# Performance work log

Hardware: AMD Instinct MI355X
Metric: run time of the kernel (lower is better)

Reference implementation:

```python
import jax, jax.numpy as jnp
import numpy as np

N, E = 50000, 800000
IN_CH, HID, OUT = 128, 64, 64
H1, H2 = 4, 1
NEG_SLOPE = 0.2  # PyG GATConv default


def _glorot(key, shape):
    fan_in, fan_out = shape[0], shape[-1]
    lim = (6.0 / (fan_in + fan_out)) ** 0.5
    return jax.random.uniform(key, shape, jnp.float32, -lim, lim)


def setup_inputs() -> dict:
    key = jax.random.key(0)
    ks = jax.random.split(key, 12)
    x = jax.random.normal(ks[0], (N, IN_CH), jnp.float32)
    edge_index = jax.random.randint(ks[1], (2, E), 0, N, jnp.int64)
    # layer 1: in_ch -> hid, 4 heads, concat
    W1 = _glorot(ks[2], (IN_CH, H1 * HID))
    a_src1 = _glorot(ks[3], (H1, HID))
    a_dst1 = _glorot(ks[4], (H1, HID))
    b1 = jnp.zeros((H1 * HID,), jnp.float32)
    # layer 2: hid*4 -> out, 1 head, mean (concat=False)
    W2 = _glorot(ks[5], (H1 * HID, H2 * OUT))
    a_src2 = _glorot(ks[6], (H2, OUT))
    a_dst2 = _glorot(ks[7], (H2, OUT))
    b2 = jnp.zeros((OUT,), jnp.float32)
    return {"x": x, "edge_index": edge_index, "W1": W1, "a_src1": a_src1,
            "a_dst1": a_dst1, "b1": b1, "W2": W2, "a_src2": a_src2,
            "a_dst2": a_dst2, "b2": b2}


def gat_layer(x, src, dst, W, a_src, a_dst, b, concat):
    n = x.shape[0]
    Hh, Fh = a_src.shape
    h = (x @ W).reshape(n, Hh, Fh)                      # [N,H,F]
    al_src = jnp.sum(h * a_src[None], axis=-1)          # [N,H]
    al_dst = jnp.sum(h * a_dst[None], axis=-1)          # [N,H]
    logits = jax.nn.leaky_relu(al_src[src] + al_dst[dst], NEG_SLOPE)  # [E,H]
    # numerically stable segment softmax over destination nodes
    mx = jax.ops.segment_max(logits, dst, num_segments=n)
    mx = jnp.where(jnp.isfinite(mx), mx, 0.0)
    e = jnp.exp(logits - mx[dst])                       # [E,H]
    denom = jax.ops.segment_sum(e, dst, num_segments=n)  # [N,H]
    alpha = e / jnp.maximum(denom[dst], 1e-16)          # [E,H]
    msg = h[src] * alpha[:, :, None]                    # [E,H,F]
    out = jax.ops.segment_sum(msg, dst, num_segments=n)  # [N,H,F]
    out = out.reshape(n, Hh * Fh) if concat else out.mean(axis=1)
    return out + b


def reference(x, edge_index, W1, a_src1, a_dst1, b1, W2, a_src2, a_dst2, b2):
    n = x.shape[0]
    # PyG GATConv adds self-loops by default
    loops = jnp.arange(n, dtype=edge_index.dtype)
    src = jnp.concatenate([edge_index[0], loops])
    dst = jnp.concatenate([edge_index[1], loops])
    h = gat_layer(x, src, dst, W1, a_src1, a_dst1, b1, concat=True)
    h = jax.nn.elu(h)
    # dropout is identity in eval mode
    out = gat_layer(h, src, dst, W2, a_src2, a_dst2, b2, concat=False)
    return out
```

## Files before the change

kernel.cpp:

```cpp
#include <hip/hip_runtime.h>
#include <math.h>

#define NEG_SLOPE 0.2f
#define SLOTS 64
#define PARTB 256

typedef unsigned short ushort_t;
typedef _Float16 f16x8 __attribute__((ext_vector_type(8)));
typedef _Float16 h2v  __attribute__((ext_vector_type(2)));
typedef float f32x4v __attribute__((ext_vector_type(4)));

__device__ __forceinline__ float leaky(float x) { return x > 0.f ? x : NEG_SLOPE * x; }

__device__ __forceinline__ ushort_t f2h(float f) {
    union { _Float16 h; ushort_t u; } v; v.h = (_Float16)f; return v.u;
}
__device__ __forceinline__ unsigned packh(float a, float b) {
    union { h2v h; unsigned u; } c; c.h[0] = (_Float16)a; c.h[1] = (_Float16)b; return c.u;
}

__global__ __launch_bounds__(256) void k_prep0(const float* __restrict__ W1, const float* __restrict__ W2,
                                               const float* __restrict__ as1, const float* __restrict__ ad1,
                                               const float* __restrict__ as2, const float* __restrict__ ad2,
                                               ushort_t* __restrict__ W1t, ushort_t* __restrict__ W2t,
                                               float* __restrict__ va1s, float* __restrict__ va1d,
                                               float* __restrict__ va2s, float* __restrict__ va2d) {
    int b = blockIdx.x, t = threadIdx.x;
    if (b < 256) {
        if (t < 128) W1t[b * 128 + t] = f2h(W1[t * 256 + b]);
    } else if (b < 320) {
        int n = b - 256;
        W2t[n * 256 + t] = f2h(W2[t * 64 + n]);
    } else if (b == 320) {
        for (int idx = t; idx < 1024; idx += 256) {
            int k = idx >> 3, h = (idx >> 1) & 3, sd = idx & 1;
            const float* a = sd ? ad1 : as1;
            float acc = 0.f;
            for (int f = 0; f < 64; ++f) acc += W1[k * 256 + h * 64 + f] * a[h * 64 + f];
            (sd ? va1d : va1s)[k * 4 + h] = acc;
        }
    } else {
        for (int idx = t; idx < 512; idx += 256) {
            int k = idx >> 1, sd = idx & 1;
            const float* a = sd ? ad2 : as2;
            float acc = 0.f;
            for (int f = 0; f < 64; ++f) acc += W2[k * 64 + f] * a[f];
            (sd ? va2d : va2s)[k] = acc;
        }
    }
}

__global__ __launch_bounds__(256) void k_partA(const int* __restrict__ ei, int E, int CH, int NBKT,
                                               int* __restrict__ bcnt) {
    __shared__ int hist[256];
    int k = blockIdx.x, t = threadIdx.x;
    hist[t] = 0;
    __syncthreads();
    int i0 = k * CH;
    for (int it = 0; it < CH; it += 256) {
        int i = i0 + it + t;
        if (it + t < CH && i < E) {
            int d = ei[E + i];
            atomicAdd(&hist[d >> 8], 1);
        }
    }
    __syncthreads();
    if (t < NBKT) bcnt[t * PARTB + k] = hist[t];
}

__global__ __launch_bounds__(256) void k_partB1(const int* __restrict__ bcnt,
                                                int* __restrict__ offs, int* __restrict__ btot) {
    __shared__ int wsum[4];
    int t = threadIdx.x, b = blockIdx.x;
    int c = bcnt[b * PARTB + t];
    int lane = t & 63, w = t >> 6;
    int v = c;
    #pragma unroll
    for (int off = 1; off < 64; off <<= 1) {
        int u = __shfl_up(v, off, 64);
        if (lane >= off) v += u;
    }
    if (lane == 63) wsum[w] = v;
    __syncthreads();
    int add = 0;
    for (int ww = 0; ww < w; ++ww) add += wsum[ww];
    offs[b * PARTB + t] = v - c + add;
    if (t == 255) btot[b] = v + add;
}

__global__ __launch_bounds__(256) void k_partB2(const int* __restrict__ btot,
                                                int* __restrict__ bstart, int NBKT, int E) {
    __shared__ int wsum[4];
    int t = threadIdx.x;
    int c = (t < NBKT) ? btot[t] : 0;
    int lane = t & 63, w = t >> 6;
    int v = c;
    #pragma unroll
    for (int off = 1; off < 64; off <<= 1) {
        int u = __shfl_up(v, off, 64);
        if (lane >= off) v += u;
    }
    if (lane == 63) wsum[w] = v;
    __syncthreads();
    int add = 0;
    for (int ww = 0; ww < w; ++ww) add += wsum[ww];
    if (t < NBKT) bstart[t] = v - c + add;
    if (t == 0) bstart[NBKT] = E;
}

__global__ __launch_bounds__(256) void k_partC(const int* __restrict__ ei, int E, int CH, int NBKT,
                                               const int* __restrict__ offs, const int* __restrict__ bstart,
                                               unsigned* __restrict__ epk) {
    __shared__ int cur[256];
    int k = blockIdx.x, t = threadIdx.x;
    if (t < NBKT) cur[t] = bstart[t] + offs[t * PARTB + k];
    __syncthreads();
    int i0 = k * CH;
    for (int it = 0; it < CH; it += 256) {
        int i = i0 + it + t;
        if (it + t < CH && i < E) {
            unsigned s = (unsigned)ei[i];
            unsigned d = (unsigned)ei[E + i];
            int pos = atomicAdd(&cur[d >> 8], 1);
            epk[pos] = (d << 16) | s;
        }
    }
}

__global__ __launch_bounds__(256) void k_partD(const unsigned* __restrict__ epk, const int* __restrict__ bstart,
                                               int* __restrict__ cnt, ushort_t* __restrict__ csr, int N) {
    __shared__ ushort_t rows[256 * SLOTS];
    __shared__ int cl[256];
    int b = blockIdx.x, t = threadIdx.x;
    for (int i = t; i < 256 * SLOTS / 8; i += 256)
        *(uint4*)&rows[(size_t)i * 8] = make_uint4(0, 0, 0, 0);
    cl[t] = 0;
    __syncthreads();
    int n0 = b * 256;
    if (n0 + t < N) rows[t * SLOTS] = (ushort_t)(n0 + t);
    int e0 = bstart[b], e1 = bstart[b + 1];
    for (int i = e0 + t; i < e1; i += 256) {
        unsigned u = epk[i];
        int dl = (u >> 16) & 255;
        int slot = atomicAdd(&cl[dl], 1);
        if (slot < SLOTS - 1) rows[dl * SLOTS + 1 + slot] = (ushort_t)(u & 0xFFFFu);
    }
    __syncthreads();
    int nvalid = N - n0; if (nvalid > 256) nvalid = 256;
    size_t gbase = (size_t)n0 * SLOTS;
    for (int i = t; i < nvalid * SLOTS / 8; i += 256)
        *(uint4*)(csr + gbase + (size_t)i * 8) = *(const uint4*)&rows[(size_t)i * 8];
    if (t < nvalid) {
        int c = cl[t]; if (c > SLOTS - 1) c = SLOTS - 1;
        cnt[n0 + t] = c;
    }
}

__global__ __launch_bounds__(256) void k_prep1x(const float* __restrict__ x,
                                                const float* __restrict__ va1s, const float* __restrict__ va1d,
                                                ushort_t* __restrict__ xh,
                                                float4* __restrict__ alS, float4* __restrict__ alD, int N) {
    int b = blockIdx.x, t = threadIdx.x;
    int r = b * 16 + (t >> 4);
    int idx = t & 15;
    if (r >= N) return;
    const float* xr = x + (size_t)r * 128 + idx * 8;
    float4 f0 = *(const float4*)xr;
    float4 f1 = *(const float4*)(xr + 4);
    uint4 pv;
    pv.x = packh(f0.x, f0.y); pv.y = packh(f0.z, f0.w);
    pv.z = packh(f1.x, f1.y); pv.w = packh(f1.z, f1.w);
    *(uint4*)&xh[(size_t)r * 128 + idx * 8] = pv;
    float xs[8] = {f0.x, f0.y, f0.z, f0.w, f1.x, f1.y, f1.z, f1.w};
    float s0 = 0, s1 = 0, s2 = 0, s3 = 0, d0 = 0, d1 = 0, d2 = 0, d3 = 0;
    #pragma unroll
    for (int j = 0; j < 8; ++j) {
        int k = idx * 8 + j;
        float4 vs = *(const float4*)&va1s[k * 4];
        float4 vd = *(const float4*)&va1d[k * 4];
        s0 += xs[j] * vs.x; s1 += xs[j] * vs.y; s2 += xs[j] * vs.z; s3 += xs[j] * vs.w;
        d0 += xs[j] * vd.x; d1 += xs[j] * vd.y; d2 += xs[j] * vd.z; d3 += xs[j] * vd.w;
    }
    #pragma unroll
    for (int off = 8; off >= 1; off >>= 1) {
        s0 += __shfl_xor(s0, off, 64); s1 += __shfl_xor(s1, off, 64);
        s2 += __shfl_xor(s2, off, 64); s3 += __shfl_xor(s3, off, 64);
        d0 += __shfl_xor(d0, off, 64); d1 += __shfl_xor(d1, off, 64);
        d2 += __shfl_xor(d2, off, 64); d3 += __shfl_xor(d3, off, 64);
    }
    if (idx == 0) {
        alS[r] = make_float4(s0, s1, s2, s3);
        alD[r] = make_float4(d0, d1, d2, d3);
    }
}

#define CONS(p, a) do { \
    _Float16 ah_ = (_Float16)(a); \
    h2v a2_ = {ah_, ah_}; \
    union { uint4 u; h2v h[4]; } c_; c_.u = (p); \
    ha0 += c_.h[0] * a2_; ha1 += c_.h[1] * a2_; \
    ha2 += c_.h[2] * a2_; ha3 += c_.h[3] * a2_; } while (0)

#define FLUSH() do { \
    acc[0] += (float)ha0[0]; acc[1] += (float)ha0[1]; \
    acc[2] += (float)ha1[0]; acc[3] += (float)ha1[1]; \
    acc[4] += (float)ha2[0]; acc[5] += (float)ha2[1]; \
    acc[6] += (float)ha3[0]; acc[7] += (float)ha3[1]; \
    ha0 = (h2v)0; ha1 = (h2v)0; ha2 = (h2v)0; ha3 = (h2v)0; } while (0)

__global__ __launch_bounds__(256) void k_agg1(const int* __restrict__ cnt, const ushort_t* __restrict__ csr,
                                              const float4* __restrict__ alS4, const float4* __restrict__ alD4,
                                              const ushort_t* __restrict__ xh,
                                              ushort_t* __restrict__ aggh, int N) {
    __shared__ float s_alpha[4][SLOTS][4];
    __shared__ int   s_off[4][SLOTS];
    int w = threadIdx.x >> 6, lane = threadIdx.x & 63;
    int n = blockIdx.x * 4 + w;
    if (n >= N) return;
    int stored = cnt[n]; if (stored > SLOTS - 1) stored = SLOTS - 1;
    int deg = stored + 1;
    int s = 0;
    if (lane < deg) s = csr[(size_t)n * SLOTS + lane];
    s_off[w][lane] = (lane < deg) ? (s << 8) : 0;

    float e0 = 0.f, e1 = 0.f, e2 = 0.f, e3 = 0.f;
    if (lane < deg) {
        float4 ald = alD4[n];
        float4 as = alS4[s];
        e0 = __expf(leaky(as.x + ald.x));
        e1 = __expf(leaky(as.y + ald.y));
        e2 = __expf(leaky(as.z + ald.z));
        e3 = __expf(leaky(as.w + ald.w));
    }
    *(float4*)&s_alpha[w][lane][0] = make_float4(e0, e1, e2, e3);

    int head = lane >> 4, cid = lane & 15;
    const char* xb = (const char*)xh + cid * 16;

    float acc[8];
    #pragma unroll
    for (int i = 0; i < 8; ++i) acc[i] = 0.f;
    h2v ha0 = (h2v)0, ha1 = (h2v)0, ha2 = (h2v)0, ha3 = (h2v)0;

    int nit = (deg + 3) & ~3;

    int4 ovA = *(const int4*)&s_off[w][0];
    uint4 pA0 = *(const uint4*)(xb + ovA.x);
    uint4 pA1 = *(const uint4*)(xb + ovA.y);
    uint4 pA2 = *(const uint4*)(xb + ovA.z);
    uint4 pA3 = *(const uint4*)(xb + ovA.w);

    for (int j = 0; j < nit; j += 8) {
        uint4 pB0, pB1, pB2, pB3;
        bool hasB = (j + 4 < nit);
        if (hasB) {
            int4 ovB = *(const int4*)&s_off[w][j + 4];
            pB0 = *(const uint4*)(xb + ovB.x);
            pB1 = *(const uint4*)(xb + ovB.y);
            pB2 = *(const uint4*)(xb + ovB.z);
            pB3 = *(const uint4*)(xb + ovB.w);
        }
        {
            float a0 = s_alpha[w][j + 0][head];
            float a1 = s_alpha[w][j + 1][head];
            float a2 = s_alpha[w][j + 2][head];
            float a3 = s_alpha[w][j + 3][head];
            CONS(pA0, a0); CONS(pA1, a1); CONS(pA2, a2); CONS(pA3, a3);
        }
        if (hasB) {
            if (j + 8 < nit) {
                int4 ovA2 = *(const int4*)&s_off[w][j + 8];
                pA0 = *(const uint4*)(xb + ovA2.x);
                pA1 = *(const uint4*)(xb + ovA2.y);
                pA2 = *(const uint4*)(xb + ovA2.z);
                pA3 = *(const uint4*)(xb + ovA2.w);
            }
            float a0 = s_alpha[w][j + 4][head];
            float a1 = s_alpha[w][j + 5][head];
            float a2 = s_alpha[w][j + 6][head];
            float a3 = s_alpha[w][j + 7][head];
            CONS(pB0, a0); CONS(pB1, a1); CONS(pB2, a2); CONS(pB3, a3);
        }
        FLUSH();
    }

    float d0 = e0, d1 = e1, d2 = e2, d3 = e3;
    #pragma unroll
    for (int off = 32; off >= 1; off >>= 1) {
        d0 += __shfl_xor(d0, off, 64); d1 += __shfl_xor(d1, off, 64);
        d2 += __shfl_xor(d2, off, 64); d3 += __shfl_xor(d3, off, 64);
    }
    float dh = head == 0 ? d0 : head == 1 ? d1 : head == 2 ? d2 : d3;
    float inv = 1.f / fmaxf(dh, 1e-16f);

    uint4 u;
    u.x = packh(acc[0] * inv, acc[1] * inv);
    u.y = packh(acc[2] * inv, acc[3] * inv);
    u.z = packh(acc[4] * inv, acc[5] * inv);
    u.w = packh(acc[6] * inv, acc[7] * inv);
    *(uint4*)(aggh + (size_t)n * 512 + head * 128 + cid * 8) = u;
}
#undef CONS
#undef FLUSH

__global__ __launch_bounds__(256) void k_gemmO(const ushort_t* __restrict__ aggh, const ushort_t* __restrict__ W1t,
                                               const ushort_t* __restrict__ W2t,
                                               const float* __restrict__ b1,
                                               const float* __restrict__ va2s, const float* __restrict__ va2d,
                                               ushort_t* __restrict__ h2h,
                                               float* __restrict__ al2S, float* __restrict__ al2D, int N) {
    __shared__ ushort_t sU[4 * 32 * 136];
    __shared__ float s_al2w[4][32][2];
    int t = threadIdx.x;
    int w = t >> 6, lane = t & 63;
    int m = lane & 15, quad = lane >> 4;
    int r0 = blockIdx.x * 32;

    #pragma unroll
    for (int q = 0; q < 8; ++q) {
        int idx = t + q * 256;
        int row = idx >> 6, off = idx & 63;
        int gr = r0 + row;
        uint4 v = (gr < N) ? *(const uint4*)(aggh + (size_t)gr * 512 + off * 8)
                           : make_uint4(0, 0, 0, 0);
        int h = off >> 4, k8 = off & 15;
        *(uint4*)&sU[(size_t)(h * 32 + row) * 136 + k8 * 8] = v;
    }
    __syncthreads();

    f32x4v acc[2][4];
    #pragma unroll
    for (int r = 0; r < 2; ++r)
        #pragma unroll
        for (int cg = 0; cg < 4; ++cg) acc[r][cg] = (f32x4v){0.f, 0.f, 0.f, 0.f};
    #pragma unroll
    for (int ks = 0; ks < 4; ++ks) {
        f16x8 af[2];
        #pragma unroll
        for (int r = 0; r < 2; ++r)
            af[r] = *(f16x8*)&sU[(size_t)(w * 32 + r * 16 + m) * 136 + ks * 32 + quad * 8];
        #pragma unroll
        for (int cg = 0; cg < 4; ++cg) {
            f16x8 bf = *(f16x8*)&W1t[(size_t)(w * 64 + cg * 16 + m) * 128 + ks * 32 + quad * 8];
            #pragma unroll
            for (int r = 0; r < 2; ++r)
                acc[r][cg] = __builtin_amdgcn_mfma_f32_16x16x32_f16(af[r], bf, acc[r][cg], 0, 0, 0);
        }
    }
    __syncthreads();

    ushort_t* sO = sU;
    float ps[2][4], pd[2][4];
    #pragma unroll
    for (int r = 0; r < 2; ++r)
        #pragma unroll
        for (int reg = 0; reg < 4; ++reg) { ps[r][reg] = 0.f; pd[r][reg] = 0.f; }
    #pragma unroll
    for (int cg = 0; cg < 4; ++cg) {
        int c = w * 64 + cg * 16 + m;
        float bias = b1[c];
        float v2s = va2s[c], v2d = va2d[c];
        #pragma unroll
        for (int r = 0; r < 2; ++r)
            #pragma unroll
            for (int reg = 0; reg < 4; ++reg) {
                int row = r * 16 + quad * 4 + reg;
                float v = acc[r][cg][reg] + bias;
                v = v > 0.f ? v : (__expf(v) - 1.f);
                sO[(size_t)row * 264 + c] = f2h(v);
                ps[r][reg] += v * v2s;
                pd[r][reg] += v * v2d;
            }
    }
    #pragma unroll
    for (int off = 1; off <= 8; off <<= 1)
        #pragma unroll
        for (int r = 0; r < 2; ++r)
            #pragma unroll
            for (int reg = 0; reg < 4; ++reg) {
                ps[r][reg] += __shfl_xor(ps[r][reg], off, 64);
                pd[r][reg] += __shfl_xor(pd[r][reg], off, 64);
            }
    if (m == 0) {
        #pragma unroll
        for (int r = 0; r < 2; ++r)
            #pragma unroll
            for (int reg = 0; reg < 4; ++reg) {
                int row = r * 16 + quad * 4 + reg;
                s_al2w[w][row][0] = ps[r][reg];
                s_al2w[w][row][1] = pd[r][reg];
            }
    }
    __syncthreads();

    if (t < 32) {
        int gr = r0 + t;
        if (gr < N) {
            float a = 0.f, b = 0.f;
            #pragma unroll
            for (int w2 = 0; w2 < 4; ++w2) { a += s_al2w[w2][t][0]; b += s_al2w[w2][t][1]; }
            al2S[gr] = a; al2D[gr] = b;
        }
    }

    f32x4v acc2[2];
    #pragma unroll
    for (int r = 0; r < 2; ++r) acc2[r] = (f32x4v){0.f, 0.f, 0.f, 0.f};
    #pragma unroll
    for (int kb = 0; kb < 2; ++kb)
        #pragma unroll
        for (int ks = 0; ks < 4; ++ks) {
            int kk = kb * 128 + ks * 32 + quad * 8;
            f16x8 bf = *(f16x8*)&W2t[(size_t)(w * 16 + m) * 256 + kk];
            #pragma unroll
            for (int r = 0; r < 2; ++r) {
                f16x8 af = *(f16x8*)&sO[(size_t)(r * 16 + m) * 264 + kk];
                acc2[r] = __builtin_amdgcn_mfma_f32_16x16x32_f16(af, bf, acc2[r], 0, 0, 0);
            }
        }
    int col = w * 16 + m;
    #pragma unroll
    for (int r = 0; r < 2; ++r) {
        int gr0 = r0 + r * 16 + quad * 4;
        #pragma unroll
        for (int reg = 0; reg < 4; ++reg) {
            int gr = gr0 + reg;
            if (gr < N) h2h[(size_t)gr * 64 + col] = f2h(acc2[r][reg]);
        }
    }
}

__global__ __launch_bounds__(256) void k_agg2(const int* __restrict__ cnt, const ushort_t* __restrict__ csr,
                                              const float* __restrict__ alS, const float* __restrict__ alD,
                                              const ushort_t* __restrict__ h2h, const float* __restrict__ b2,
                                              float* __restrict__ out, int N) {
    int lane = threadIdx.x & 63;
    int n = blockIdx.x * 4 + (threadIdx.x >> 6);
    if (n >= N) return;
    int stored = cnt[n]; if (stored > SLOTS - 1) stored = SLOTS - 1;
    int deg = stored + 1;
    const ushort_t* crow = csr + (size_t)n * SLOTS;

    int s0 = 0;
    if (lane < deg) s0 = crow[lane];

    int grp = lane >> 3, cid = lane & 7;
    int choff = cid * 16;
    const char* hbase = (const char*)h2h;

    uint4 pbuf[3];
    #pragma unroll
    for (int i = 0; i < 3; ++i) {
        int sj = __shfl(s0, i * 8 + grp, 64);
        pbuf[i] = *(const uint4*)(hbase + ((size_t)sj << 7) + choff);
    }

    float ald = alD[n];
    float e0 = 0.f;
    if (lane < deg) e0 = __expf(leaky(alS[s0] + ald));

    h2v ha0 = (h2v)0, ha1 = (h2v)0, ha2 = (h2v)0, ha3 = (h2v)0;
    #pragma unroll
    for (int i = 0; i < 3; ++i) {
        float a = __shfl(e0, i * 8 + grp, 64);
        union { uint4 u; h2v h[4]; } c; c.u = pbuf[i];
        _Float16 ah = (_Float16)a;
        h2v a2 = {ah, ah};
        ha0 += c.h[0] * a2; ha1 += c.h[1] * a2;
        ha2 += c.h[2] * a2; ha3 += c.h[3] * a2;
    }
    for (int j = 24; j < deg; j += 8) {
        int jj = j + grp;
        float a = __shfl(e0, jj, 64);
        int sj = __shfl(s0, jj, 64);
        union { uint4 u; h2v h[4]; } c;
        c.u = *(const uint4*)(hbase + ((size_t)sj << 7) + choff);
        _Float16 ah = (_Float16)a;
        h2v a2 = {ah, ah};
        ha0 += c.h[0] * a2; ha1 += c.h[1] * a2;
        ha2 += c.h[2] * a2; ha3 += c.h[3] * a2;
    }

    float den = e0;
    #pragma unroll
    for (int off = 32; off >= 1; off >>= 1) den += __shfl_xor(den, off, 64);
    float inv = 1.f / fmaxf(den, 1e-16f);

    float acc[8];
    acc[0] = (float)ha0[0]; acc[1] = (float)ha0[1];
    acc[2] = (float)ha1[0]; acc[3] = (float)ha1[1];
    acc[4] = (float)ha2[0]; acc[5] = (float)ha2[1];
    acc[6] = (float)ha3[0]; acc[7] = (float)ha3[1];
    #pragma unroll
    for (int off = 8; off <= 32; off <<= 1)
        #pragma unroll
        for (int i = 0; i < 8; ++i) acc[i] += __shfl_xor(acc[i], off, 64);

    if (grp == 0) {
        int c8 = cid * 8;
        float4 b0 = *(const float4*)&b2[c8];
        float4 b1v = *(const float4*)&b2[c8 + 4];
        float4 o0 = make_float4(acc[0]*inv + b0.x, acc[1]*inv + b0.y, acc[2]*inv + b0.z, acc[3]*inv + b0.w);
        float4 o1 = make_float4(acc[4]*inv + b1v.x, acc[5]*inv + b1v.y, acc[6]*inv + b1v.z, acc[7]*inv + b1v.w);
        *(float4*)(out + (size_t)n * 64 + c8) = o0;
        *(float4*)(out + (size_t)n * 64 + c8 + 4) = o1;
    }
}

extern "C" void kernel_launch(void* const* d_in, const int* in_sizes, int n_in,
                              void* d_out, int out_size, void* d_ws, size_t ws_size,
                              hipStream_t stream) {
    const float* x      = (const float*)d_in[0];
    const int*   ei     = (const int*)d_in[1];
    const float* W1     = (const float*)d_in[2];
    const float* a_src1 = (const float*)d_in[3];
    const float* a_dst1 = (const float*)d_in[4];
    const float* b1     = (const float*)d_in[5];
    const float* W2     = (const float*)d_in[6];
    const float* a_src2 = (const float*)d_in[7];
    const float* a_dst2 = (const float*)d_in[8];
    const float* b2     = (const float*)d_in[9];
    float* out = (float*)d_out;

    int N = in_sizes[0] / 128;
    int E = in_sizes[1] / 2;

    char* ws = (char*)d_ws;
    size_t off = 0;
    auto alloc = [&](size_t bytes) -> void* {
        void* p = ws + off;
        off = (off + bytes + 255) & ~(size_t)255;
        return p;
    };
    ushort_t* xh    = (ushort_t*)alloc((size_t)N * 128 * 2);
    ushort_t* aggh  = (ushort_t*)alloc((size_t)N * 512 * 2);
    ushort_t* h2h   = (ushort_t*)alloc((size_t)N * 64 * 2);
    ushort_t* W1t   = (ushort_t*)alloc(256 * 128 * 2);
    ushort_t* W2t   = (ushort_t*)alloc(64 * 256 * 2);
    float* va1s  = (float*)alloc(128 * 4 * 4);
    float* va1d  = (float*)alloc(128 * 4 * 4);
    float* va2s  = (float*)alloc(256 * 4);
    float* va2d  = (float*)alloc(256 * 4);
    float* alS1  = (float*)alloc((size_t)N * 4 * 4);
    float* alD1  = (float*)alloc((size_t)N * 4 * 4);
    float* alS2  = (float*)alloc((size_t)N * 4);
    float* alD2  = (float*)alloc((size_t)N * 4);
    int*   cnt   = (int*)alloc((size_t)N * 4);
    ushort_t* csr = (ushort_t*)alloc((size_t)N * SLOTS * 2);
    int NBKT = (N + 255) >> 8;
    int*      bcnt  = (int*)alloc((size_t)NBKT * PARTB * 4);
    int*      offs  = (int*)alloc((size_t)NBKT * PARTB * 4);
    int*      btot  = (int*)alloc((size_t)NBKT * 4);
    int*      bstart= (int*)alloc((size_t)(NBKT + 1) * 4);
    unsigned* epk   = (unsigned*)alloc((size_t)E * 4);
    (void)ws_size; (void)n_in; (void)out_size;

    int CH  = (E + PARTB - 1) / PARTB;
    int XB  = (N + 15) / 16;
    int AB1 = (N + 3) / 4;
    int GO  = (N + 31) / 32;
    int NC4 = (N + 3) / 4;

    k_prep0<<<322, 256, 0, stream>>>(W1, W2, a_src1, a_dst1, a_src2, a_dst2,
                                     W1t, W2t, va1s, va1d, va2s, va2d);
    k_partA<<<PARTB, 256, 0, stream>>>(ei, E, CH, NBKT, bcnt);
    k_partB1<<<NBKT, 256, 0, stream>>>(bcnt, offs, btot);
    k_partB2<<<1, 256, 0, stream>>>(btot, bstart, NBKT, E);
    k_partC<<<PARTB, 256, 0, stream>>>(ei, E, CH, NBKT, offs, bstart, epk);
    k_partD<<<NBKT, 256, 0, stream>>>(epk, bstart, cnt, csr, N);
    k_prep1x<<<XB, 256, 0, stream>>>(x, va1s, va1d, xh, (float4*)alS1, (float4*)alD1, N);
    k_agg1<<<AB1, 256, 0, stream>>>(cnt, csr,
                                    (const float4*)alS1, (const float4*)alD1,
                                    xh, aggh, N);
    k_gemmO<<<GO, 256, 0, stream>>>(aggh, W1t, W2t, b1, va2s, va2d,
                                    h2h, alS2, alD2, N);
    k_agg2<<<NC4, 256, 0, stream>>>(cnt, csr, alS2, alD2, h2h, b2, out, N);
}
```

Measured before the change: 241.9 us.

## Merge independent prep kernels and split fused GEMM into two kernels

Merges the edge-histogram pass into the weight-prep kernel and the x-to-half/attention-logit pass into the edge-scatter kernel, so independent work shares launches and fills the GPU together. The fused layer-1 projection plus layer-2 GEMM kernel is split in two: the first writes the ELU output to a new global half buffer, and the second runs a separate 64-row tiled GEMM with W2 staged in shared memory. This removes launch gaps and may improve occupancy or tiling of the second GEMM, at the cost of an extra global round trip of N x 256 half values and one more launch.

```diff
diff --git a/kernel.cpp b/kernel.cpp
--- a/kernel.cpp
+++ b/kernel.cpp
@@ -19,13 +19,29 @@
     union { h2v h; unsigned u; } c; c.h[0] = (_Float16)a; c.h[1] = (_Float16)b; return c.u;
 }
 
-__global__ __launch_bounds__(256) void k_prep0(const float* __restrict__ W1, const float* __restrict__ W2,
-                                               const float* __restrict__ as1, const float* __restrict__ ad1,
-                                               const float* __restrict__ as2, const float* __restrict__ ad2,
-                                               ushort_t* __restrict__ W1t, ushort_t* __restrict__ W2t,
-                                               float* __restrict__ va1s, float* __restrict__ va1d,
-                                               float* __restrict__ va2s, float* __restrict__ va2d) {
+__global__ __launch_bounds__(256) void k_prep0A(const float* __restrict__ W1, const float* __restrict__ W2,
+                                                const float* __restrict__ as1, const float* __restrict__ ad1,
+                                                const float* __restrict__ as2, const float* __restrict__ ad2,
+                                                ushort_t* __restrict__ W1t, ushort_t* __restrict__ W2t,
+                                                float* __restrict__ va1s, float* __restrict__ va1d,
+                                                float* __restrict__ va2s, float* __restrict__ va2d,
+                                                const int* __restrict__ ei, int E, int CH, int NBKT,
+                                                int* __restrict__ bcnt) {
+    __shared__ int hist[256];
     int b = blockIdx.x, t = threadIdx.x;
+    if (b >= 322) {
+        int k = b - 322;
+        hist[t] = 0;
+        __syncthreads();
+        int i0 = k * CH;
+        for (int it = 0; it < CH; it += 256) {
+            int i = i0 + it + t;
+            if (it + t < CH && i < E) atomicAdd(&hist[ei[E + i] >> 8], 1);
+        }
+        __syncthreads();
+        if (t < NBKT) bcnt[t * PARTB + k] = hist[t];
+        return;
+    }
     if (b < 256) {
         if (t < 128) W1t[b * 128 + t] = f2h(W1[t * 256 + b]);
     } else if (b < 320) {
@@ -50,24 +66,6 @@
     }
 }
 
-__global__ __launch_bounds__(256) void k_partA(const int* __restrict__ ei, int E, int CH, int NBKT,
-                                               int* __restrict__ bcnt) {
-    __shared__ int hist[256];
-    int k = blockIdx.x, t = threadIdx.x;
-    hist[t] = 0;
-    __syncthreads();
-    int i0 = k * CH;
-    for (int it = 0; it < CH; it += 256) {
-        int i = i0 + it + t;
-        if (it + t < CH && i < E) {
-            int d = ei[E + i];
-            atomicAdd(&hist[d >> 8], 1);
-        }
-    }
-    __syncthreads();
-    if (t < NBKT) bcnt[t * PARTB + k] = hist[t];
-}
-
 __global__ __launch_bounds__(256) void k_partB1(const int* __restrict__ bcnt,
                                                 int* __restrict__ offs, int* __restrict__ btot) {
     __shared__ int wsum[4];
@@ -108,22 +106,62 @@
     if (t == 0) bstart[NBKT] = E;
 }
 
-__global__ __launch_bounds__(256) void k_partC(const int* __restrict__ ei, int E, int CH, int NBKT,
-                                               const int* __restrict__ offs, const int* __restrict__ bstart,
-                                               unsigned* __restrict__ epk) {
+__global__ __launch_bounds__(256) void k_partCx(const int* __restrict__ ei, int E, int CH, int NBKT,
+                                                const int* __restrict__ offs, const int* __restrict__ bstart,
+                                                unsigned* __restrict__ epk,
+                                                const float* __restrict__ x,
+                                                const float* __restrict__ va1s, const float* __restrict__ va1d,
+                                                ushort_t* __restrict__ xh,
+                                                float4* __restrict__ alS, float4* __restrict__ alD, int N) {
     __shared__ int cur[256];
-    int k = blockIdx.x, t = threadIdx.x;
-    if (t < NBKT) cur[t] = bstart[t] + offs[t * PARTB + k];
-    __syncthreads();
-    int i0 = k * CH;
-    for (int it = 0; it < CH; it += 256) {
-        int i = i0 + it + t;
-        if (it + t < CH && i < E) {
-            unsigned s = (unsigned)ei[i];
-            unsigned d = (unsigned)ei[E + i];
-            int pos = atomicAdd(&cur[d >> 8], 1);
-            epk[pos] = (d << 16) | s;
-        }
+    int b = blockIdx.x, t = threadIdx.x;
+    if (b < PARTB) {
+        int k = b;
+        if (t < NBKT) cur[t] = bstart[t] + offs[t * PARTB + k];
+        __syncthreads();
+        int i0 = k * CH;
+        for (int it = 0; it < CH; it += 256) {
+            int i = i0 + it + t;
+            if (it + t < CH && i < E) {
+                unsigned s = (unsigned)ei[i];
+                unsigned d = (unsigned)ei[E + i];
+                int pos = atomicAdd(&cur[d >> 8], 1);
+                epk[pos] = (d << 16) | s;
+            }
+        }
+        return;
+    }
+    int bb = b - PARTB;
+    int r = bb * 16 + (t >> 4);
+    int idx = t & 15;
+    if (r >= N) return;
+    const float* xr = x + (size_t)r * 128 + idx * 8;
+    float4 f0 = *(const float4*)xr;
+    float4 f1 = *(const float4*)(xr + 4);
+    uint4 pv;
+    pv.x = packh(f0.x, f0.y); pv.y = packh(f0.z, f0.w);
+    pv.z = packh(f1.x, f1.y); pv.w = packh(f1.z, f1.w);
+    *(uint4*)&xh[(size_t)r * 128 + idx * 8] = pv;
+    float xs[8] = {f0.x, f0.y, f0.z, f0.w, f1.x, f1.y, f1.z, f1.w};
+    float s0 = 0, s1 = 0, s2 = 0, s3 = 0, d0 = 0, d1 = 0, d2 = 0, d3 = 0;
+    #pragma unroll
+    for (int j = 0; j < 8; ++j) {
+        int k = idx * 8 + j;
+        float4 vs = *(const float4*)&va1s[k * 4];
+        float4 vd = *(const float4*)&va1d[k * 4];
+        s0 += xs[j] * vs.x; s1 += xs[j] * vs.y; s2 += xs[j] * vs.z; s3 += xs[j] * vs.w;
+        d0 += xs[j] * vd.x; d1 += xs[j] * vd.y; d2 += xs[j] * vd.z; d3 += xs[j] * vd.w;
+    }
+    #pragma unroll
+    for (int off = 8; off >= 1; off >>= 1) {
+        s0 += __shfl_xor(s0, off, 64); s1 += __shfl_xor(s1, off, 64);
+        s2 += __shfl_xor(s2, off, 64); s3 += __shfl_xor(s3, off, 64);
+        d0 += __shfl_xor(d0, off, 64); d1 += __shfl_xor(d1, off, 64);
+        d2 += __shfl_xor(d2, off, 64); d3 += __shfl_xor(d3, off, 64);
+    }
+    if (idx == 0) {
+        alS[r] = make_float4(s0, s1, s2, s3);
+        alD[r] = make_float4(d0, d1, d2, d3);
     }
 }
 
@@ -156,44 +194,6 @@
     }
 }
 
-__global__ __launch_bounds__(256) void k_prep1x(const float* __restrict__ x,
-                                                const float* __restrict__ va1s, const float* __restrict__ va1d,
-                                                ushort_t* __restrict__ xh,
-                                                float4* __restrict__ alS, float4* __restrict__ alD, int N) {
-    int b = blockIdx.x, t = threadIdx.x;
-    int r = b * 16 + (t >> 4);
-    int idx = t & 15;
-    if (r >= N) return;
-    const float* xr = x + (size_t)r * 128 + idx * 8;
-    float4 f0 = *(const float4*)xr;
-    float4 f1 = *(const float4*)(xr + 4);
-    uint4 pv;
-    pv.x = packh(f0.x, f0.y); pv.y = packh(f0.z, f0.w);
-    pv.z = packh(f1.x, f1.y); pv.w = packh(f1.z, f1.w);
-    *(uint4*)&xh[(size_t)r * 128 + idx * 8] = pv;
-    float xs[8] = {f0.x, f0.y, f0.z, f0.w, f1.x, f1.y, f1.z, f1.w};
-    float s0 = 0, s1 = 0, s2 = 0, s3 = 0, d0 = 0, d1 = 0, d2 = 0, d3 = 0;
-    #pragma unroll
-    for (int j = 0; j < 8; ++j) {
-        int k = idx * 8 + j;
-        float4 vs = *(const float4*)&va1s[k * 4];
-        float4 vd = *(const float4*)&va1d[k * 4];
-        s0 += xs[j] * vs.x; s1 += xs[j] * vs.y; s2 += xs[j] * vs.z; s3 += xs[j] * vs.w;
-        d0 += xs[j] * vd.x; d1 += xs[j] * vd.y; d2 += xs[j] * vd.z; d3 += xs[j] * vd.w;
-    }
-    #pragma unroll
-    for (int off = 8; off >= 1; off >>= 1) {
-        s0 += __shfl_xor(s0, off, 64); s1 += __shfl_xor(s1, off, 64);
-        s2 += __shfl_xor(s2, off, 64); s3 += __shfl_xor(s3, off, 64);
-        d0 += __shfl_xor(d0, off, 64); d1 += __shfl_xor(d1, off, 64);
-        d2 += __shfl_xor(d2, off, 64); d3 += __shfl_xor(d3, off, 64);
-    }
-    if (idx == 0) {
-        alS[r] = make_float4(s0, s1, s2, s3);
-        alD[r] = make_float4(d0, d1, d2, d3);
-    }
-}
-
 #define CONS(p, a) do { \
     _Float16 ah_ = (_Float16)(a); \
     h2v a2_ = {ah_, ah_}; \
@@ -303,12 +303,11 @@
 #undef CONS
 #undef FLUSH
 
-__global__ __launch_bounds__(256) void k_gemmO(const ushort_t* __restrict__ aggh, const ushort_t* __restrict__ W1t,
-                                               const ushort_t* __restrict__ W2t,
-                                               const float* __restrict__ b1,
-                                               const float* __restrict__ va2s, const float* __restrict__ va2d,
-                                               ushort_t* __restrict__ h2h,
-                                               float* __restrict__ al2S, float* __restrict__ al2D, int N) {
+__global__ __launch_bounds__(256) void k_g1(const ushort_t* __restrict__ aggh, const ushort_t* __restrict__ W1t,
+                                            const float* __restrict__ b1,
+                                            const float* __restrict__ va2s, const float* __restrict__ va2d,
+                                            ushort_t* __restrict__ out1h,
+                                            float* __restrict__ al2S, float* __restrict__ al2D, int N) {
     __shared__ ushort_t sU[4 * 32 * 136];
     __shared__ float s_al2w[4][32][2];
     int t = threadIdx.x;
@@ -347,9 +346,7 @@
                 acc[r][cg] = __builtin_amdgcn_mfma_f32_16x16x32_f16(af[r], bf, acc[r][cg], 0, 0, 0);
         }
     }
-    __syncthreads();
-
-    ushort_t* sO = sU;
+
     float ps[2][4], pd[2][4];
     #pragma unroll
     for (int r = 0; r < 2; ++r)
@@ -365,9 +362,10 @@
             #pragma unroll
             for (int reg = 0; reg < 4; ++reg) {
                 int row = r * 16 + quad * 4 + reg;
+                int gr = r0 + row;
                 float v = acc[r][cg][reg] + bias;
                 v = v > 0.f ? v : (__expf(v) - 1.f);
-                sO[(size_t)row * 264 + c] = f2h(v);
+                if (gr < N) out1h[(size_t)gr * 256 + c] = f2h(v);
                 ps[r][reg] += v * v2s;
                 pd[r][reg] += v * v2d;
             }
@@ -392,7 +390,6 @@
             }
     }
     __syncthreads();
-
     if (t < 32) {
         int gr = r0 + t;
         if (gr < N) {
@@ -402,30 +399,58 @@
             al2S[gr] = a; al2D[gr] = b;
         }
     }
-
-    f32x4v acc2[2];
-    #pragma unroll
-    for (int r = 0; r < 2; ++r) acc2[r] = (f32x4v){0.f, 0.f, 0.f, 0.f};
-    #pragma unroll
-    for (int kb = 0; kb < 2; ++kb)
+}
+
+__global__ __launch_bounds__(256) void k_g2(const ushort_t* __restrict__ in, const ushort_t* __restrict__ W2t,
+                                            ushort_t* __restrict__ h2h, int N) {
+    __shared__ ushort_t As[64 * 136];
+    __shared__ ushort_t Bs[64 * 136];
+    int t = threadIdx.x;
+    int r0 = blockIdx.x * 64;
+    int w = t >> 6, lane = t & 63;
+    int m = lane & 15, quad = lane >> 4;
+    f32x4v acc[4];
+    #pragma unroll
+    for (int r = 0; r < 4; ++r) acc[r] = (f32x4v){0.f, 0.f, 0.f, 0.f};
+    for (int kb = 0; kb < 2; ++kb) {
+        #pragma unroll
+        for (int q = 0; q < 4; ++q) {
+            int idx = t + q * 256;
+            int row = idx >> 4, off = idx & 15;
+            int gr = r0 + row;
+            uint4 v = (gr < N) ? *(const uint4*)(in + (size_t)gr * 256 + kb * 128 + off * 8)
+                               : make_uint4(0, 0, 0, 0);
+            *(uint4*)&As[row * 136 + off * 8] = v;
+        }
+        #pragma unroll
+        for (int q = 0; q < 4; ++q) {
+            int idx = t + q * 256;
+            int row = idx >> 4, off = idx & 15;
+            uint4 v = *(const uint4*)(W2t + (size_t)row * 256 + kb * 128 + off * 8);
+            *(uint4*)&Bs[row * 136 + off * 8] = v;
+        }
+        __syncthreads();
         #pragma unroll
         for (int ks = 0; ks < 4; ++ks) {
-            int kk = kb * 128 + ks * 32 + quad * 8;
-            f16x8 bf = *(f16x8*)&W2t[(size_t)(w * 16 + m) * 256 + kk];
+            int k0 = ks * 32 + quad * 8;
+            f16x8 af[4], bfr;
             #pragma unroll
-            for (int r = 0; r < 2; ++r) {
-                f16x8 af = *(f16x8*)&sO[(size_t)(r * 16 + m) * 264 + kk];
-                acc2[r] = __builtin_amdgcn_mfma_f32_16x16x32_f16(af, bf, acc2[r], 0, 0, 0);
-            }
-        }
+            for (int r = 0; r < 4; ++r) af[r] = *(f16x8*)&As[(r * 16 + m) * 136 + k0];
+            bfr = *(f16x8*)&Bs[(w * 16 + m) * 136 + k0];
+            #pragma unroll
+            for (int r = 0; r < 4; ++r)
+                acc[r] = __builtin_amdgcn_mfma_f32_16x16x32_f16(af[r], bfr, acc[r], 0, 0, 0);
+        }
+        __syncthreads();
+    }
     int col = w * 16 + m;
     #pragma unroll
-    for (int r = 0; r < 2; ++r) {
+    for (int r = 0; r < 4; ++r) {
         int gr0 = r0 + r * 16 + quad * 4;
         #pragma unroll
         for (int reg = 0; reg < 4; ++reg) {
             int gr = gr0 + reg;
-            if (gr < N) h2h[(size_t)gr * 64 + col] = f2h(acc2[r][reg]);
+            if (gr < N) h2h[(size_t)gr * 64 + col] = f2h(acc[r][reg]);
         }
     }
 }
@@ -534,6 +559,7 @@
     };
     ushort_t* xh    = (ushort_t*)alloc((size_t)N * 128 * 2);
     ushort_t* aggh  = (ushort_t*)alloc((size_t)N * 512 * 2);
+    ushort_t* out1h = (ushort_t*)alloc((size_t)N * 256 * 2);
     ushort_t* h2h   = (ushort_t*)alloc((size_t)N * 64 * 2);
     ushort_t* W1t   = (ushort_t*)alloc(256 * 128 * 2);
     ushort_t* W2t   = (ushort_t*)alloc(64 * 256 * 2);
@@ -558,21 +584,22 @@
     int CH  = (E + PARTB - 1) / PARTB;
     int XB  = (N + 15) / 16;
     int AB1 = (N + 3) / 4;
-    int GO  = (N + 31) / 32;
+    int G1  = (N + 31) / 32;
+    int G2  = (N + 63) / 64;
     int NC4 = (N + 3) / 4;
 
-    k_prep0<<<322, 256, 0, stream>>>(W1, W2, a_src1, a_dst1, a_src2, a_dst2,
-                                     W1t, W2t, va1s, va1d, va2s, va2d);
-    k_partA<<<PARTB, 256, 0, stream>>>(ei, E, CH, NBKT, bcnt);
+    k_prep0A<<<322 + PARTB, 256, 0, stream>>>(W1, W2, a_src1, a_dst1, a_src2, a_dst2,
+                                              W1t, W2t, va1s, va1d, va2s, va2d,
+                                              ei, E, CH, NBKT, bcnt);
     k_partB1<<<NBKT, 256, 0, stream>>>(bcnt, offs, btot);
     k_partB2<<<1, 256, 0, stream>>>(btot, bstart, NBKT, E);
-    k_partC<<<PARTB, 256, 0, stream>>>(ei, E, CH, NBKT, offs, bstart, epk);
+    k_partCx<<<PARTB + XB, 256, 0, stream>>>(ei, E, CH, NBKT, offs, bstart, epk,
+                                             x, va1s, va1d, xh, (float4*)alS1, (float4*)alD1, N);
     k_partD<<<NBKT, 256, 0, stream>>>(epk, bstart, cnt, csr, N);
-    k_prep1x<<<XB, 256, 0, stream>>>(x, va1s, va1d, xh, (float4*)alS1, (float4*)alD1, N);
     k_agg1<<<AB1, 256, 0, stream>>>(cnt, csr,
                                     (const float4*)alS1, (const float4*)alD1,
                                     xh, aggh, N);
-    k_gemmO<<<GO, 256, 0, stream>>>(aggh, W1t, W2t, b1, va2s, va2d,
-                                    h2h, alS2, alD2, N);
+    k_g1<<<G1, 256, 0, stream>>>(aggh, W1t, b1, va2s, va2d, out1h, alS2, alD2, N);
+    k_g2<<<G2, 256, 0, stream>>>(out1h, W2t, h2h, N);
     k_agg2<<<NC4, 256, 0, stream>>>(cnt, csr, alS2, alD2, h2h, b2, out, N);
 }
```

After: 238.6 us. Within noise of the previous version (-1.4%).
